# Kernel tuning notes

Hardware: AMD Instinct MI355X
Metric: run time of the kernel (lower is better)

## Reference

```python
import jax, jax.numpy as jnp
import numpy as np

D = 512      # d_model
H = 8        # nhead
HD = D // H  # head dim
L = 8        # axis-0 length (torch seq dim, batch_first=False)
S = 128      # axis-1 length (torch batch dim; relation-tensor axis)
NL = 3       # encoder layers
EPS = 1e-5


def setup_inputs() -> dict:
    key = jax.random.key(0)
    ks = jax.random.split(key, 16)
    w = lambda k, shape: jax.random.normal(k, shape, jnp.float32) * 0.02
    return {
        "x": jax.random.normal(ks[0], (L, S, D), jnp.float32),
        # stacked per-layer transformer params (leading dim = NL)
        "attn_in_w": w(ks[1], (NL, 3 * D, D)), "attn_in_b": jnp.zeros((NL, 3 * D), jnp.float32),
        "attn_out_w": w(ks[2], (NL, D, D)),    "attn_out_b": jnp.zeros((NL, D), jnp.float32),
        "ln1_w": jnp.ones((NL, D), jnp.float32), "ln1_b": jnp.zeros((NL, D), jnp.float32),
        "ln2_w": jnp.ones((NL, D), jnp.float32), "ln2_b": jnp.zeros((NL, D), jnp.float32),
        "ff1_w": w(ks[3], (NL, 4 * D, D)), "ff1_b": jnp.zeros((NL, 4 * D), jnp.float32),
        "ff2_w": w(ks[4], (NL, D, 4 * D)), "ff2_b": jnp.zeros((NL, D), jnp.float32),
        "fln_w": jnp.ones((D,), jnp.float32), "fln_b": jnp.zeros((D,), jnp.float32),
        # 4 projection MLPs stacked: 0=sub, 1=obj, 2=verb_sub, 3=verb_obj
        "mlp_w0": w(ks[5], (4, D, D)), "mlp_b0": jnp.zeros((4, D), jnp.float32),
        "mlp_w1": w(ks[6], (4, D, D)), "mlp_b1": jnp.zeros((4, D), jnp.float32),
        "mlp_w2": w(ks[7], (4, D, D)), "mlp_b2": jnp.zeros((4, D), jnp.float32),
    }


def _ln(x, w, b):
    m = jnp.mean(x, axis=-1, keepdims=True)
    v = jnp.mean(jnp.square(x - m), axis=-1, keepdims=True)
    return (x - m) * jax.lax.rsqrt(v + EPS) * w + b


def _mha(x, in_w, in_b, out_w, out_b):
    # x: (L, B, D); attention over axis 0 (torch batch_first=False semantics)
    l, b, _ = x.shape
    qkv = x @ in_w.T + in_b                      # (L, B, 3D)
    q, k, v = jnp.split(qkv, 3, axis=-1)
    q = q.reshape(l, b, H, HD)
    k = k.reshape(l, b, H, HD)
    v = v.reshape(l, b, H, HD)
    scores = jnp.einsum("lbhd,mbhd->bhlm", q, k) / jnp.sqrt(jnp.float32(HD))
    attn = jax.nn.softmax(scores, axis=-1)
    o = jnp.einsum("bhlm,mbhd->lbhd", attn, v).reshape(l, b, D)
    return o @ out_w.T + out_b


def _mlp(x, w0, b0, w1, b1, w2, b2):
    h = jax.nn.relu(x @ w0.T + b0)
    h = jax.nn.relu(h @ w1.T + b1)
    return h @ w2.T + b2


def _forward(x, attn_in_w, attn_in_b, attn_out_w, attn_out_b,
             ln1_w, ln1_b, ln2_w, ln2_b, ff1_w, ff1_b, ff2_w, ff2_b,
             fln_w, fln_b, mlp_w0, mlp_b0, mlp_w1, mlp_b1, mlp_w2, mlp_b2):
    # TransformerEncoder (post-norm, relu, no dropout at eval)
    h = x
    for i in range(NL):
        h = _ln(h + _mha(h, attn_in_w[i], attn_in_b[i], attn_out_w[i], attn_out_b[i]),
                ln1_w[i], ln1_b[i])
        ff = jax.nn.relu(h @ ff1_w[i].T + ff1_b[i]) @ ff2_w[i].T + ff2_b[i]
        h = _ln(h + ff, ln2_w[i], ln2_b[i])
    h = _ln(h, fln_w, fln_b)  # final encoder norm

    sub = _mlp(h, mlp_w0[0], mlp_b0[0], mlp_w1[0], mlp_b1[0], mlp_w2[0], mlp_b2[0])
    obj = _mlp(h, mlp_w0[1], mlp_b0[1], mlp_w1[1], mlp_b1[1], mlp_w2[1], mlp_b2[1])
    vsub = _mlp(h, mlp_w0[2], mlp_b0[2], mlp_w1[2], mlp_b1[2], mlp_w2[2], mlp_b2[2])
    vobj = _mlp(h, mlp_w0[3], mlp_b0[3], mlp_w1[3], mlp_b1[3], mlp_w2[3], mlp_b2[3])

    # sub.unsqueeze(1) * vsub.unsqueeze(2): (B0, S, S, D)
    sub4 = sub[:, None, :, :] * vsub[:, :, None, :]
    obj4 = obj[:, None, :, :] * vobj[:, :, None, :]
    # p_x = sub4 @ obj4.transpose(-2, -1): (B0, S, S, S)
    return jnp.einsum("bijd,bikd->bijk", sub4, obj4)


def reference(x, attn_in_w, attn_in_b, attn_out_w, attn_out_b,
              ln1_w, ln1_b, ln2_w, ln2_b, ff1_w, ff1_b, ff2_w, ff2_b,
              fln_w, fln_b, mlp_w0, mlp_b0, mlp_w1, mlp_b1, mlp_w2, mlp_b2):
    return _forward(x, attn_in_w, attn_in_b, attn_out_w, attn_out_b,
                    ln1_w, ln1_b, ln2_w, ln2_b, ff1_w, ff1_b, ff2_w, ff2_b,
                    fln_w, fln_b, mlp_w0, mlp_b0, mlp_w1, mlp_b1, mlp_w2, mlp_b2)
```

## Files before the change

### kernel.cpp

```cpp
#include <hip/hip_runtime.h>
#include <hip/hip_bf16.h>

#define DEV __device__ __forceinline__

typedef __attribute__((ext_vector_type(8))) short bf16x8;
typedef __attribute__((ext_vector_type(8))) unsigned short u16x8;
typedef __attribute__((ext_vector_type(4))) float f32x4;

DEV unsigned short f2bf(float f) {
  return __builtin_bit_cast(unsigned short, __float2bfloat16(f));
}
DEV float bf2f(unsigned short h) { return __uint_as_float(((unsigned int)h) << 16); }

DEV int swz(int row, int byteoff) { return row * 128 + (byteoff ^ ((row & 7) << 4)); }

__global__ void cvt_kernel(const float* __restrict__ src, unsigned short* __restrict__ dst,
                           float* __restrict__ dstf, int n) {
  long i = ((long)blockIdx.x * blockDim.x + threadIdx.x) * 8;
  long stride = (long)gridDim.x * blockDim.x * 8;
  for (; i < n; i += stride) {
    f32x4 a = *(const f32x4*)(src + i);
    f32x4 b = *(const f32x4*)(src + i + 4);
    u16x8 o;
    o[0] = f2bf(a[0]); o[1] = f2bf(a[1]); o[2] = f2bf(a[2]); o[3] = f2bf(a[3]);
    o[4] = f2bf(b[0]); o[5] = f2bf(b[1]); o[6] = f2bf(b[2]); o[7] = f2bf(b[3]);
    *(u16x8*)(dst + i) = o;
    if (dstf) { *(f32x4*)(dstf + i) = a; *(f32x4*)(dstf + i + 4) = b; }
  }
}

struct CvtJobs { const float* s[7]; unsigned short* d[7]; int n[7]; };
__global__ void cvtw_kernel(CvtJobs J) {
  const int seg = blockIdx.y;
  const float* __restrict__ src = J.s[seg];
  unsigned short* __restrict__ dst = J.d[seg];
  const int n = J.n[seg];
  long i = ((long)blockIdx.x * blockDim.x + threadIdx.x) * 8;
  long stride = (long)gridDim.x * blockDim.x * 8;
  for (; i < n; i += stride) {
    f32x4 a = *(const f32x4*)(src + i);
    f32x4 b = *(const f32x4*)(src + i + 4);
    u16x8 o;
    o[0] = f2bf(a[0]); o[1] = f2bf(a[1]); o[2] = f2bf(a[2]); o[3] = f2bf(a[3]);
    o[4] = f2bf(b[0]); o[5] = f2bf(b[1]); o[6] = f2bf(b[2]); o[7] = f2bf(b[3]);
    *(u16x8*)(dst + i) = o;
  }
}

template <int BM, int ACT, int WF32, int WBF>
__global__ __launch_bounds__(256) void gemm_kernel(
    const unsigned short* __restrict__ X, const unsigned short* __restrict__ Wt,
    const float* __restrict__ bias, float* Yf, unsigned short* __restrict__ Ybf,
    int M, int N, int K, long xbs, long wbs, long bbs, long ybs) {
  constexpr int CA = (BM * 64) / (256 * 8);
  constexpr int ABY = BM * 64 * 2;
  constexpr int BBY = 64 * 64 * 2;
  constexpr int MI = BM / 32;
  __shared__ __align__(16) char Asb[2 * ABY];
  __shared__ __align__(16) char Bsb[2 * BBY];
  const int t = threadIdx.x;
  const int bn = blockIdx.x, bm = blockIdx.y, bz = blockIdx.z;
  const unsigned short* Xp = X + (long)bz * xbs;
  const unsigned short* Wp = Wt + (long)bz * wbs;

  const int lane = t & 63, wv = t >> 6;
  const int wr = wv >> 1, wc = wv & 1;
  f32x4 acc[MI][2] = {};

  int rowA[CA], slotA[CA], rowB[2], slotB[2];
#pragma unroll
  for (int c = 0; c < CA; ++c) { int id = c * 256 + t; rowA[c] = id >> 3; slotA[c] = id & 7; }
#pragma unroll
  for (int c = 0; c < 2; ++c) { int id = c * 256 + t; rowB[c] = id >> 3; slotB[c] = id & 7; }

  u16x8 ra[CA], rb[2];
  auto load = [&](int kt) {
#pragma unroll
    for (int c = 0; c < CA; ++c)
      ra[c] = *(const u16x8*)(Xp + (long)(bm * BM + rowA[c]) * K + kt + slotA[c] * 8);
#pragma unroll
    for (int c = 0; c < 2; ++c)
      rb[c] = *(const u16x8*)(Wp + (long)(bn * 64 + rowB[c]) * K + kt + slotB[c] * 8);
  };
  auto store = [&](int cur) {
#pragma unroll
    for (int c = 0; c < CA; ++c)
      *(u16x8*)(Asb + cur * ABY + swz(rowA[c], slotA[c] * 16)) = ra[c];
#pragma unroll
    for (int c = 0; c < 2; ++c)
      *(u16x8*)(Bsb + cur * BBY + swz(rowB[c], slotB[c] * 16)) = rb[c];
  };

  const int NT = K >> 6;
  load(0);
  store(0);
  load(64);
  __syncthreads();
  for (int ki = 0; ki < NT; ++ki) {
    const int cur = ki & 1;
    if (ki + 1 < NT) store(cur ^ 1);
    if (ki + 2 < NT) load((ki + 2) << 6);
#pragma unroll
    for (int kk = 0; kk < 2; ++kk) {
      const int kb = kk * 64 + ((lane >> 4) << 4);
      bf16x8 af[MI], bfv[2];
#pragma unroll
      for (int mi = 0; mi < MI; ++mi)
        af[mi] = *(const bf16x8*)(Asb + cur * ABY + swz(wr * (MI * 16) + mi * 16 + (lane & 15), kb));
#pragma unroll
      for (int ni = 0; ni < 2; ++ni)
        bfv[ni] = *(const bf16x8*)(Bsb + cur * BBY + swz(wc * 32 + ni * 16 + (lane & 15), kb));
#pragma unroll
      for (int mi = 0; mi < MI; ++mi)
#pragma unroll
        for (int ni = 0; ni < 2; ++ni)
          acc[mi][ni] = __builtin_amdgcn_mfma_f32_16x16x32_bf16(af[mi], bfv[ni], acc[mi][ni], 0, 0, 0);
    }
    __syncthreads();
  }
#pragma unroll
  for (int ni = 0; ni < 2; ++ni) {
    const int n = bn * 64 + wc * 32 + ni * 16 + (lane & 15);
    const float bv = bias[(long)bz * bbs + n];
#pragma unroll
    for (int mi = 0; mi < MI; ++mi) {
#pragma unroll
      for (int rr = 0; rr < 4; ++rr) {
        const int gm = bm * BM + wr * (MI * 16) + mi * 16 + ((lane >> 4) << 2) + rr;
        float v = acc[mi][ni][rr] + bv;
        if (ACT == 1) v = fmaxf(v, 0.f);
        const long o = (long)bz * ybs + (long)gm * N + n;
        if (WF32) Yf[o] = v;
        if (WBF) Ybf[o] = f2bf(v);
      }
    }
  }
}

__global__ __launch_bounds__(256) void attn_kernel(const unsigned short* __restrict__ qkv,
                                                   unsigned short* __restrict__ o) {
  __shared__ float P[512];
  const int s = blockIdx.x;
  const int t = threadIdx.x;
#pragma unroll
  for (int rep = 0; rep < 2; ++rep) {
    const int idx = t + rep * 256;
    const int h = idx >> 6, l = (idx >> 3) & 7, m = idx & 7;
    const unsigned short* qp = qkv + (long)(l * 128 + s) * 1536 + h * 64;
    const unsigned short* kp = qkv + (long)(m * 128 + s) * 1536 + 512 + h * 64;
    float acc = 0.f;
#pragma unroll
    for (int c = 0; c < 64; c += 8) {
      u16x8 q8 = *(const u16x8*)(qp + c);
      u16x8 k8 = *(const u16x8*)(kp + c);
#pragma unroll
      for (int j = 0; j < 8; ++j) acc += bf2f(q8[j]) * bf2f(k8[j]);
    }
    P[idx] = acc * 0.125f;
  }
  __syncthreads();
  if (t < 64) {
    const int base = t * 8;
    float mx = -1e30f;
#pragma unroll
    for (int m = 0; m < 8; ++m) mx = fmaxf(mx, P[base + m]);
    float e[8], sum = 0.f;
#pragma unroll
    for (int m = 0; m < 8; ++m) { e[m] = expf(P[base + m] - mx); sum += e[m]; }
    const float inv = 1.f / sum;
#pragma unroll
    for (int m = 0; m < 8; ++m) P[base + m] = e[m] * inv;
  }
  __syncthreads();
#pragma unroll
  for (int rep = 0; rep < 16; ++rep) {
    const int idx = t + rep * 256;
    const int d = idx & 63, h = (idx >> 6) & 7, l = idx >> 9;
    float acc = 0.f;
#pragma unroll
    for (int m = 0; m < 8; ++m)
      acc += P[h * 64 + l * 8 + m] * bf2f(qkv[(long)(m * 128 + s) * 1536 + 1024 + h * 64 + d]);
    o[(long)(l * 128 + s) * 512 + h * 64 + d] = f2bf(acc);
  }
}

template <int RES, int WF32>
__global__ __launch_bounds__(256) void ln_kernel(const float* a, const float* res,
                                                 const float* __restrict__ w,
                                                 const float* __restrict__ bb, float* hf,
                                                 unsigned short* __restrict__ hbf) {
  __shared__ float red[8];
  const int row = blockIdx.x, t = threadIdx.x;
  const long base = (long)row * 512;
  float x0 = a[base + t], x1 = a[base + t + 256];
  if (RES) { x0 += res[base + t]; x1 += res[base + t + 256]; }
  float s = x0 + x1;
#pragma unroll
  for (int msk = 32; msk; msk >>= 1) s += __shfl_xor(s, msk, 64);
  if ((t & 63) == 0) red[t >> 6] = s;
  __syncthreads();
  const float mean = (red[0] + red[1] + red[2] + red[3]) * (1.f / 512.f);
  const float d0 = x0 - mean, d1 = x1 - mean;
  float v = d0 * d0 + d1 * d1;
#pragma unroll
  for (int msk = 32; msk; msk >>= 1) v += __shfl_xor(v, msk, 64);
  if ((t & 63) == 0) red[4 + (t >> 6)] = v;
  __syncthreads();
  const float var = (red[4] + red[5] + red[6] + red[7]) * (1.f / 512.f);
  const float inv = rsqrtf(var + 1e-5f);
  const float o0 = d0 * inv * w[t] + bb[t];
  const float o1 = d1 * inv * w[t + 256] + bb[t + 256];
  if (WF32) { hf[base + t] = o0; hf[base + t + 256] = o1; }
  hbf[base + t] = f2bf(o0);
  hbf[base + t + 256] = f2bf(o1);
}

__global__ __launch_bounds__(256) void phasec_kernel(const float* __restrict__ subp,
                                                     const unsigned short* __restrict__ objbf,
                                                     const float* __restrict__ vsub,
                                                     const float* __restrict__ vobj,
                                                     float* __restrict__ out) {
  constexpr int ABY = 128 * 64 * 2;
  __shared__ __align__(16) char Asb[2 * ABY];
  __shared__ __align__(16) char Bsb[2 * ABY];
  __shared__ float Wl[512];
  const int t = threadIdx.x;
  const int i = blockIdx.x, b = blockIdx.y;
  const long base_bi = ((long)b * 128 + i) * 512;
  for (int d = t; d < 512; d += 256) Wl[d] = vsub[base_bi + d] * vobj[base_bi + d];

  const int lane = t & 63, wv = t >> 6;
  const int wr = wv >> 1, wc = wv & 1;
  f32x4 acc[4][4] = {};

  int row[4], slot[4];
#pragma unroll
  for (int c = 0; c < 4; ++c) { int id = c * 256 + t; row[c] = id >> 3; slot[c] = id & 7; }

  f32x4 fa[4][2];
  u16x8 rb[4];
  auto load = [&](int kt) {
#pragma unroll
    for (int c = 0; c < 4; ++c) {
      const long g = ((long)b * 128 + row[c]) * 512 + kt + slot[c] * 8;
      fa[c][0] = *(const f32x4*)(subp + g);
      fa[c][1] = *(const f32x4*)(subp + g + 4);
      rb[c] = *(const u16x8*)(objbf + g);
    }
  };
  auto store = [&](int cur, int ktd) {
#pragma unroll
    for (int c = 0; c < 4; ++c) {
      const float* wp = Wl + ktd + slot[c] * 8;
      f32x4 w0 = *(const f32x4*)wp;
      f32x4 w1 = *(const f32x4*)(wp + 4);
      u16x8 oa;
      oa[0] = f2bf(fa[c][0][0] * w0[0]); oa[1] = f2bf(fa[c][0][1] * w0[1]);
      oa[2] = f2bf(fa[c][0][2] * w0[2]); oa[3] = f2bf(fa[c][0][3] * w0[3]);
      oa[4] = f2bf(fa[c][1][0] * w1[0]); oa[5] = f2bf(fa[c][1][1] * w1[1]);
      oa[6] = f2bf(fa[c][1][2] * w1[2]); oa[7] = f2bf(fa[c][1][3] * w1[3]);
      *(u16x8*)(Asb + cur * ABY + swz(row[c], slot[c] * 16)) = oa;
      *(u16x8*)(Bsb + cur * ABY + swz(row[c], slot[c] * 16)) = rb[c];
    }
  };

  __syncthreads();
  load(0);
  store(0, 0);
  load(64);
  __syncthreads();
  for (int ki = 0; ki < 8; ++ki) {
    const int cur = ki & 1;
    if (ki + 1 < 8) store(cur ^ 1, (ki + 1) * 64);
    if (ki + 2 < 8) load((ki + 2) * 64);
#pragma unroll
    for (int kk = 0; kk < 2; ++kk) {
      const int kb = kk * 64 + ((lane >> 4) << 4);
      bf16x8 af[4], bfv[4];
#pragma unroll
      for (int mi = 0; mi < 4; ++mi)
        af[mi] = *(const bf16x8*)(Asb + cur * ABY + swz(wr * 64 + mi * 16 + (lane & 15), kb));
#pragma unroll
      for (int ni = 0; ni < 4; ++ni)
        bfv[ni] = *(const bf16x8*)(Bsb + cur * ABY + swz(wc * 64 + ni * 16 + (lane & 15), kb));
#pragma unroll
      for (int mi = 0; mi < 4; ++mi)
#pragma unroll
        for (int ni = 0; ni < 4; ++ni)
          acc[mi][ni] = __builtin_amdgcn_mfma_f32_16x16x32_bf16(af[mi], bfv[ni], acc[mi][ni], 0, 0, 0);
    }
    __syncthreads();
  }
  float* ob = out + ((long)b * 128 + i) * 128 * 128;
#pragma unroll
  for (int mi = 0; mi < 4; ++mi) {
#pragma unroll
    for (int rr = 0; rr < 4; ++rr) {
      const int j = wr * 64 + mi * 16 + ((lane >> 4) << 2) + rr;
      float* orow = ob + (long)j * 128 + wc * 64 + (lane & 15);
#pragma unroll
      for (int ni = 0; ni < 4; ++ni) orow[ni * 16] = acc[mi][ni][rr];
    }
  }
}

extern "C" void kernel_launch(void* const* d_in, const int* in_sizes, int n_in, void* d_out,
                              int out_size, void* d_ws, size_t ws_size, hipStream_t stream) {
  const float* x          = (const float*)d_in[0];
  const float* attn_in_w  = (const float*)d_in[1];
  const float* attn_in_b  = (const float*)d_in[2];
  const float* attn_out_w = (const float*)d_in[3];
  const float* attn_out_b = (const float*)d_in[4];
  const float* ln1_w = (const float*)d_in[5];
  const float* ln1_b = (const float*)d_in[6];
  const float* ln2_w = (const float*)d_in[7];
  const float* ln2_b = (const float*)d_in[8];
  const float* ff1_w = (const float*)d_in[9];
  const float* ff1_b = (const float*)d_in[10];
  const float* ff2_w = (const float*)d_in[11];
  const float* ff2_b = (const float*)d_in[12];
  const float* fln_w = (const float*)d_in[13];
  const float* fln_b = (const float*)d_in[14];
  const float* mlp_w0 = (const float*)d_in[15];
  const float* mlp_b0 = (const float*)d_in[16];
  const float* mlp_w1 = (const float*)d_in[17];
  const float* mlp_b1 = (const float*)d_in[18];
  const float* mlp_w2 = (const float*)d_in[19];
  const float* mlp_b2 = (const float*)d_in[20];
  float* out = (float*)d_out;
  (void)in_sizes; (void)n_in; (void)out_size; (void)ws_size;

  char* ws = (char*)d_ws;
  size_t off = 0;
  auto alloc = [&](size_t bytes) -> void* {
    void* p = (void*)(ws + off);
    off += (bytes + 255) & ~(size_t)255;
    return p;
  };
  unsigned short* wq  = (unsigned short*)alloc((size_t)3 * 1536 * 512 * 2);
  unsigned short* wo  = (unsigned short*)alloc((size_t)3 * 512 * 512 * 2);
  unsigned short* wf1 = (unsigned short*)alloc((size_t)3 * 2048 * 512 * 2);
  unsigned short* wf2 = (unsigned short*)alloc((size_t)3 * 512 * 2048 * 2);
  unsigned short* wm0 = (unsigned short*)alloc((size_t)4 * 512 * 512 * 2);
  unsigned short* wm1 = (unsigned short*)alloc((size_t)4 * 512 * 512 * 2);
  unsigned short* wm2 = (unsigned short*)alloc((size_t)4 * 512 * 512 * 2);
  float* h            = (float*)alloc((size_t)1024 * 512 * 4);
  unsigned short* hbf = (unsigned short*)alloc((size_t)1024 * 512 * 2);
  unsigned short* t1  = (unsigned short*)alloc((size_t)1024 * 2048 * 2);
  float* t2           = (float*)alloc((size_t)1024 * 512 * 4);
  unsigned short* ao  = (unsigned short*)alloc((size_t)1024 * 512 * 2);
  unsigned short* z1  = (unsigned short*)alloc((size_t)4 * 1024 * 512 * 2);
  unsigned short* z2  = (unsigned short*)alloc((size_t)4 * 1024 * 512 * 2);
  float* hf4          = (float*)alloc((size_t)4 * 1024 * 512 * 4);
  unsigned short* hb4 = (unsigned short*)alloc((size_t)4 * 1024 * 512 * 2);

  CvtJobs J;
  J.s[0] = attn_in_w;  J.d[0] = wq;  J.n[0] = 3 * 1536 * 512;
  J.s[1] = attn_out_w; J.d[1] = wo;  J.n[1] = 3 * 512 * 512;
  J.s[2] = ff1_w;      J.d[2] = wf1; J.n[2] = 3 * 2048 * 512;
  J.s[3] = ff2_w;      J.d[3] = wf2; J.n[3] = 3 * 512 * 2048;
  J.s[4] = mlp_w0;     J.d[4] = wm0; J.n[4] = 4 * 512 * 512;
  J.s[5] = mlp_w1;     J.d[5] = wm1; J.n[5] = 4 * 512 * 512;
  J.s[6] = mlp_w2;     J.d[6] = wm2; J.n[6] = 4 * 512 * 512;
  cvtw_kernel<<<dim3(512, 7), 256, 0, stream>>>(J);
  cvt_kernel<<<256, 256, 0, stream>>>(x, hbf, h, 1024 * 512);

  for (int i = 0; i < 3; ++i) {
    gemm_kernel<64, 0, 0, 1><<<dim3(24, 16, 1), 256, 0, stream>>>(
        hbf, wq + (long)i * 1536 * 512, attn_in_b + i * 1536, nullptr, t1, 1024, 1536, 512, 0, 0, 0, 0);
    attn_kernel<<<128, 256, 0, stream>>>(t1, ao);
    gemm_kernel<32, 0, 1, 0><<<dim3(8, 32, 1), 256, 0, stream>>>(
        ao, wo + (long)i * 512 * 512, attn_out_b + i * 512, t2, nullptr, 1024, 512, 512, 0, 0, 0, 0);
    ln_kernel<1, 1><<<1024, 256, 0, stream>>>(t2, h, ln1_w + i * 512, ln1_b + i * 512, h, hbf);
    gemm_kernel<64, 1, 0, 1><<<dim3(32, 16, 1), 256, 0, stream>>>(
        hbf, wf1 + (long)i * 2048 * 512, ff1_b + i * 2048, nullptr, t1, 1024, 2048, 512, 0, 0, 0, 0);
    gemm_kernel<32, 0, 1, 0><<<dim3(8, 32, 1), 256, 0, stream>>>(
        t1, wf2 + (long)i * 512 * 2048, ff2_b + i * 512, t2, nullptr, 1024, 512, 2048, 0, 0, 0, 0);
    ln_kernel<1, 1><<<1024, 256, 0, stream>>>(t2, h, ln2_w + i * 512, ln2_b + i * 512, h, hbf);
  }
  ln_kernel<0, 0><<<1024, 256, 0, stream>>>(h, nullptr, fln_w, fln_b, h, hbf);

  gemm_kernel<32, 1, 0, 1><<<dim3(8, 32, 4), 256, 0, stream>>>(
      hbf, wm0, mlp_b0, nullptr, z1, 1024, 512, 512, 0, 512 * 512, 512, 1024 * 512);
  gemm_kernel<32, 1, 0, 1><<<dim3(8, 32, 4), 256, 0, stream>>>(
      z1, wm1, mlp_b1, nullptr, z2, 1024, 512, 512, 1024 * 512, 512 * 512, 512, 1024 * 512);
  gemm_kernel<32, 0, 1, 1><<<dim3(8, 32, 4), 256, 0, stream>>>(
      z2, wm2, mlp_b2, hf4, hb4, 1024, 512, 512, 1024 * 512, 512 * 512, 512, 1024 * 512);

  phasec_kernel<<<dim3(128, 8), 256, 0, stream>>>(
      hf4, hb4 + 1 * 1024 * 512, hf4 + 2L * 1024 * 512, hf4 + 3L * 1024 * 512, out);
}
```

Measured before the change: 379.6 us.

## Fuse out-proj/FF2 GEMMs with residual LayerNorm and stage phasec output through LDS

Adds a gemm_ln kernel where each block computes a full 32x512 row tile, so the residual add, bias and LayerNorm (plus the final encoder norm in the last layer) run in the GEMM epilogue. This removes the separate LN launches and the fp32 t2 round trip. The cost is that these GEMMs now launch only 32 blocks, which lowers parallelism, especially for the K=2048 FF2 step. It also merges the input conversion into the weight-conversion launch and stages the phasec output tile through LDS for coalesced float4 stores.

```diff
diff --git a/kernel.cpp b/kernel.cpp
--- a/kernel.cpp
+++ b/kernel.cpp
@@ -13,9 +13,15 @@
 DEV float bf2f(unsigned short h) { return __uint_as_float(((unsigned int)h) << 16); }
 
 DEV int swz(int row, int byteoff) { return row * 128 + (byteoff ^ ((row & 7) << 4)); }
-
-__global__ void cvt_kernel(const float* __restrict__ src, unsigned short* __restrict__ dst,
-                           float* __restrict__ dstf, int n) {
+DEV int swz32(int row, int slot) { return row * 64 + ((slot ^ ((row >> 1) & 3)) << 4); }
+
+struct CvtJobs { const float* s[8]; unsigned short* d[8]; float* df[8]; int n[8]; };
+__global__ void cvtw_kernel(CvtJobs J) {
+  const int seg = blockIdx.y;
+  const float* __restrict__ src = J.s[seg];
+  unsigned short* __restrict__ dst = J.d[seg];
+  float* __restrict__ dstf = J.df[seg];
+  const int n = J.n[seg];
   long i = ((long)blockIdx.x * blockDim.x + threadIdx.x) * 8;
   long stride = (long)gridDim.x * blockDim.x * 8;
   for (; i < n; i += stride) {
@@ -26,24 +32,6 @@
     o[4] = f2bf(b[0]); o[5] = f2bf(b[1]); o[6] = f2bf(b[2]); o[7] = f2bf(b[3]);
     *(u16x8*)(dst + i) = o;
     if (dstf) { *(f32x4*)(dstf + i) = a; *(f32x4*)(dstf + i + 4) = b; }
-  }
-}
-
-struct CvtJobs { const float* s[7]; unsigned short* d[7]; int n[7]; };
-__global__ void cvtw_kernel(CvtJobs J) {
-  const int seg = blockIdx.y;
-  const float* __restrict__ src = J.s[seg];
-  unsigned short* __restrict__ dst = J.d[seg];
-  const int n = J.n[seg];
-  long i = ((long)blockIdx.x * blockDim.x + threadIdx.x) * 8;
-  long stride = (long)gridDim.x * blockDim.x * 8;
-  for (; i < n; i += stride) {
-    f32x4 a = *(const f32x4*)(src + i);
-    f32x4 b = *(const f32x4*)(src + i + 4);
-    u16x8 o;
-    o[0] = f2bf(a[0]); o[1] = f2bf(a[1]); o[2] = f2bf(a[2]); o[3] = f2bf(a[3]);
-    o[4] = f2bf(b[0]); o[5] = f2bf(b[1]); o[6] = f2bf(b[2]); o[7] = f2bf(b[3]);
-    *(u16x8*)(dst + i) = o;
   }
 }
 
@@ -137,6 +125,175 @@
   }
 }
 
+template <int DOUBLE>
+__global__ __launch_bounds__(256) void gemm_ln_kernel(
+    const unsigned short* __restrict__ X, const unsigned short* __restrict__ Wt,
+    const float* __restrict__ bias, float* __restrict__ h,
+    unsigned short* __restrict__ hbf,
+    const float* __restrict__ g1, const float* __restrict__ b1,
+    const float* __restrict__ g2, const float* __restrict__ b2, int K) {
+  constexpr int ABY = 32 * 32 * 2;
+  constexpr int BBY = 512 * 32 * 2;
+  __shared__ __align__(16) char Asb[2 * ABY];
+  __shared__ __align__(16) char Bsb[2 * BBY];
+  __shared__ float RedS[4][32], RedQ[4][32], RedS2[4][32], RedQ2[4][32];
+  const int t = threadIdx.x;
+  const int bm = blockIdx.x;
+  const int lane = t & 63, wv = t >> 6;
+  f32x4 acc[2][8] = {};
+
+  const int arow = t >> 2, aslot = t & 3;
+  u16x8 ra, rbv[8];
+  auto load = [&](int kt) {
+    if (t < 128) ra = *(const u16x8*)(X + (long)(bm * 32 + arow) * K + kt + aslot * 8);
+#pragma unroll
+    for (int c = 0; c < 8; ++c) {
+      const int id = c * 256 + t, row = id >> 2, slot = id & 3;
+      rbv[c] = *(const u16x8*)(Wt + (long)row * K + kt + slot * 8);
+    }
+  };
+  auto store = [&](int cur) {
+    if (t < 128) *(u16x8*)(Asb + cur * ABY + swz32(arow, aslot)) = ra;
+#pragma unroll
+    for (int c = 0; c < 8; ++c) {
+      const int id = c * 256 + t, row = id >> 2, slot = id & 3;
+      *(u16x8*)(Bsb + cur * BBY + swz32(row, slot)) = rbv[c];
+    }
+  };
+
+  const int NT = K >> 5;
+  load(0);
+  store(0);
+  load(32);
+  __syncthreads();
+  for (int ki = 0; ki < NT; ++ki) {
+    const int cur = ki & 1;
+    if (ki + 1 < NT) store(cur ^ 1);
+    if (ki + 2 < NT) load((ki + 2) << 5);
+    const int ks = lane >> 4;
+    bf16x8 af[2];
+#pragma unroll
+    for (int mi = 0; mi < 2; ++mi)
+      af[mi] = *(const bf16x8*)(Asb + cur * ABY + swz32(mi * 16 + (lane & 15), ks));
+#pragma unroll
+    for (int ni = 0; ni < 8; ++ni) {
+      bf16x8 bfv = *(const bf16x8*)(Bsb + cur * BBY + swz32(wv * 128 + ni * 16 + (lane & 15), ks));
+#pragma unroll
+      for (int mi = 0; mi < 2; ++mi)
+        acc[mi][ni] = __builtin_amdgcn_mfma_f32_16x16x32_bf16(af[mi], bfv, acc[mi][ni], 0, 0, 0);
+    }
+    __syncthreads();
+  }
+
+  float ls[2][4], lq[2][4];
+#pragma unroll
+  for (int mi = 0; mi < 2; ++mi)
+#pragma unroll
+    for (int rr = 0; rr < 4; ++rr) {
+      const int gm = bm * 32 + mi * 16 + ((lane >> 4) << 2) + rr;
+      float s = 0.f, q = 0.f;
+#pragma unroll
+      for (int ni = 0; ni < 8; ++ni) {
+        const int col = wv * 128 + ni * 16 + (lane & 15);
+        float v = acc[mi][ni][rr] + bias[col] + h[(long)gm * 512 + col];
+        acc[mi][ni][rr] = v;
+        s += v; q += v * v;
+      }
+      ls[mi][rr] = s; lq[mi][rr] = q;
+    }
+#pragma unroll
+  for (int msk = 1; msk < 16; msk <<= 1)
+#pragma unroll
+    for (int mi = 0; mi < 2; ++mi)
+#pragma unroll
+      for (int rr = 0; rr < 4; ++rr) {
+        ls[mi][rr] += __shfl_xor(ls[mi][rr], msk, 64);
+        lq[mi][rr] += __shfl_xor(lq[mi][rr], msk, 64);
+      }
+  if ((lane & 15) == 0) {
+#pragma unroll
+    for (int mi = 0; mi < 2; ++mi)
+#pragma unroll
+      for (int rr = 0; rr < 4; ++rr) {
+        const int r = mi * 16 + ((lane >> 4) << 2) + rr;
+        RedS[wv][r] = ls[mi][rr];
+        RedQ[wv][r] = lq[mi][rr];
+      }
+  }
+  __syncthreads();
+#pragma unroll
+  for (int mi = 0; mi < 2; ++mi)
+#pragma unroll
+    for (int rr = 0; rr < 4; ++rr) {
+      const int r = mi * 16 + ((lane >> 4) << 2) + rr;
+      const float S = RedS[0][r] + RedS[1][r] + RedS[2][r] + RedS[3][r];
+      const float Q = RedQ[0][r] + RedQ[1][r] + RedQ[2][r] + RedQ[3][r];
+      const float mean = S * (1.f / 512.f);
+      const float var = Q * (1.f / 512.f) - mean * mean;
+      const float inv = rsqrtf(var + 1e-5f);
+      float s2 = 0.f, q2 = 0.f;
+#pragma unroll
+      for (int ni = 0; ni < 8; ++ni) {
+        const int col = wv * 128 + ni * 16 + (lane & 15);
+        float o1 = (acc[mi][ni][rr] - mean) * inv * g1[col] + b1[col];
+        acc[mi][ni][rr] = o1;
+        s2 += o1; q2 += o1 * o1;
+      }
+      ls[mi][rr] = s2; lq[mi][rr] = q2;
+    }
+  if (DOUBLE) {
+#pragma unroll
+    for (int msk = 1; msk < 16; msk <<= 1)
+#pragma unroll
+      for (int mi = 0; mi < 2; ++mi)
+#pragma unroll
+        for (int rr = 0; rr < 4; ++rr) {
+          ls[mi][rr] += __shfl_xor(ls[mi][rr], msk, 64);
+          lq[mi][rr] += __shfl_xor(lq[mi][rr], msk, 64);
+        }
+    if ((lane & 15) == 0) {
+#pragma unroll
+      for (int mi = 0; mi < 2; ++mi)
+#pragma unroll
+        for (int rr = 0; rr < 4; ++rr) {
+          const int r = mi * 16 + ((lane >> 4) << 2) + rr;
+          RedS2[wv][r] = ls[mi][rr];
+          RedQ2[wv][r] = lq[mi][rr];
+        }
+    }
+    __syncthreads();
+#pragma unroll
+    for (int mi = 0; mi < 2; ++mi)
+#pragma unroll
+      for (int rr = 0; rr < 4; ++rr) {
+        const int r = mi * 16 + ((lane >> 4) << 2) + rr;
+        const float S = RedS2[0][r] + RedS2[1][r] + RedS2[2][r] + RedS2[3][r];
+        const float Q = RedQ2[0][r] + RedQ2[1][r] + RedQ2[2][r] + RedQ2[3][r];
+        const float mean = S * (1.f / 512.f);
+        const float var = Q * (1.f / 512.f) - mean * mean;
+        const float inv = rsqrtf(var + 1e-5f);
+#pragma unroll
+        for (int ni = 0; ni < 8; ++ni) {
+          const int col = wv * 128 + ni * 16 + (lane & 15);
+          acc[mi][ni][rr] = (acc[mi][ni][rr] - mean) * inv * g2[col] + b2[col];
+        }
+      }
+  }
+#pragma unroll
+  for (int mi = 0; mi < 2; ++mi)
+#pragma unroll
+    for (int rr = 0; rr < 4; ++rr) {
+      const int gm = bm * 32 + mi * 16 + ((lane >> 4) << 2) + rr;
+#pragma unroll
+      for (int ni = 0; ni < 8; ++ni) {
+        const int col = wv * 128 + ni * 16 + (lane & 15);
+        const float v = acc[mi][ni][rr];
+        h[(long)gm * 512 + col] = v;
+        hbf[(long)gm * 512 + col] = f2bf(v);
+      }
+    }
+}
+
 __global__ __launch_bounds__(256) void attn_kernel(const unsigned short* __restrict__ qkv,
                                                    unsigned short* __restrict__ o) {
   __shared__ float P[512];
@@ -184,46 +341,16 @@
   }
 }
 
-template <int RES, int WF32>
-__global__ __launch_bounds__(256) void ln_kernel(const float* a, const float* res,
-                                                 const float* __restrict__ w,
-                                                 const float* __restrict__ bb, float* hf,
-                                                 unsigned short* __restrict__ hbf) {
-  __shared__ float red[8];
-  const int row = blockIdx.x, t = threadIdx.x;
-  const long base = (long)row * 512;
-  float x0 = a[base + t], x1 = a[base + t + 256];
-  if (RES) { x0 += res[base + t]; x1 += res[base + t + 256]; }
-  float s = x0 + x1;
-#pragma unroll
-  for (int msk = 32; msk; msk >>= 1) s += __shfl_xor(s, msk, 64);
-  if ((t & 63) == 0) red[t >> 6] = s;
-  __syncthreads();
-  const float mean = (red[0] + red[1] + red[2] + red[3]) * (1.f / 512.f);
-  const float d0 = x0 - mean, d1 = x1 - mean;
-  float v = d0 * d0 + d1 * d1;
-#pragma unroll
-  for (int msk = 32; msk; msk >>= 1) v += __shfl_xor(v, msk, 64);
-  if ((t & 63) == 0) red[4 + (t >> 6)] = v;
-  __syncthreads();
-  const float var = (red[4] + red[5] + red[6] + red[7]) * (1.f / 512.f);
-  const float inv = rsqrtf(var + 1e-5f);
-  const float o0 = d0 * inv * w[t] + bb[t];
-  const float o1 = d1 * inv * w[t + 256] + bb[t + 256];
-  if (WF32) { hf[base + t] = o0; hf[base + t + 256] = o1; }
-  hbf[base + t] = f2bf(o0);
-  hbf[base + t + 256] = f2bf(o1);
-}
-
 __global__ __launch_bounds__(256) void phasec_kernel(const float* __restrict__ subp,
                                                      const unsigned short* __restrict__ objbf,
                                                      const float* __restrict__ vsub,
                                                      const float* __restrict__ vobj,
                                                      float* __restrict__ out) {
   constexpr int ABY = 128 * 64 * 2;
-  __shared__ __align__(16) char Asb[2 * ABY];
-  __shared__ __align__(16) char Bsb[2 * ABY];
-  __shared__ float Wl[512];
+  __shared__ __align__(16) char SMEM[67584];
+  char* Asb = SMEM;
+  char* Bsb = SMEM + 2 * ABY;
+  float* Wl = (float*)(SMEM + 4 * ABY);
   const int t = threadIdx.x;
   const int i = blockIdx.x, b = blockIdx.y;
   const long base_bi = ((long)b * 128 + i) * 512;
@@ -291,16 +418,24 @@
     }
     __syncthreads();
   }
-  float* ob = out + ((long)b * 128 + i) * 128 * 128;
-#pragma unroll
-  for (int mi = 0; mi < 4; ++mi) {
+  float* C = (float*)SMEM;
+#pragma unroll
+  for (int mi = 0; mi < 4; ++mi)
 #pragma unroll
     for (int rr = 0; rr < 4; ++rr) {
       const int j = wr * 64 + mi * 16 + ((lane >> 4) << 2) + rr;
-      float* orow = ob + (long)j * 128 + wc * 64 + (lane & 15);
-#pragma unroll
-      for (int ni = 0; ni < 4; ++ni) orow[ni * 16] = acc[mi][ni][rr];
-    }
+      float* crow = C + j * 132 + wc * 64 + (lane & 15);
+#pragma unroll
+      for (int ni = 0; ni < 4; ++ni) crow[ni * 16] = acc[mi][ni][rr];
+    }
+  __syncthreads();
+  float* ob = out + ((long)b * 128 + i) * 128 * 128;
+  const int cc = (t & 31) * 4, jb = (t >> 5) * 16;
+#pragma unroll
+  for (int q = 0; q < 16; ++q) {
+    const int j = jb + q;
+    f32x4 v = *(const f32x4*)(C + j * 132 + cc);
+    *(f32x4*)(ob + (long)j * 128 + cc) = v;
   }
 }
 
@@ -347,7 +482,6 @@
   float* h            = (float*)alloc((size_t)1024 * 512 * 4);
   unsigned short* hbf = (unsigned short*)alloc((size_t)1024 * 512 * 2);
   unsigned short* t1  = (unsigned short*)alloc((size_t)1024 * 2048 * 2);
-  float* t2           = (float*)alloc((size_t)1024 * 512 * 4);
   unsigned short* ao  = (unsigned short*)alloc((size_t)1024 * 512 * 2);
   unsigned short* z1  = (unsigned short*)alloc((size_t)4 * 1024 * 512 * 2);
   unsigned short* z2  = (unsigned short*)alloc((size_t)4 * 1024 * 512 * 2);
@@ -355,6 +489,7 @@
   unsigned short* hb4 = (unsigned short*)alloc((size_t)4 * 1024 * 512 * 2);
 
   CvtJobs J;
+  for (int k = 0; k < 8; ++k) J.df[k] = nullptr;
   J.s[0] = attn_in_w;  J.d[0] = wq;  J.n[0] = 3 * 1536 * 512;
   J.s[1] = attn_out_w; J.d[1] = wo;  J.n[1] = 3 * 512 * 512;
   J.s[2] = ff1_w;      J.d[2] = wf1; J.n[2] = 3 * 2048 * 512;
@@ -362,23 +497,27 @@
   J.s[4] = mlp_w0;     J.d[4] = wm0; J.n[4] = 4 * 512 * 512;
   J.s[5] = mlp_w1;     J.d[5] = wm1; J.n[5] = 4 * 512 * 512;
   J.s[6] = mlp_w2;     J.d[6] = wm2; J.n[6] = 4 * 512 * 512;
-  cvtw_kernel<<<dim3(512, 7), 256, 0, stream>>>(J);
-  cvt_kernel<<<256, 256, 0, stream>>>(x, hbf, h, 1024 * 512);
+  J.s[7] = x;          J.d[7] = hbf; J.n[7] = 1024 * 512; J.df[7] = h;
+  cvtw_kernel<<<dim3(512, 8), 256, 0, stream>>>(J);
 
   for (int i = 0; i < 3; ++i) {
     gemm_kernel<64, 0, 0, 1><<<dim3(24, 16, 1), 256, 0, stream>>>(
         hbf, wq + (long)i * 1536 * 512, attn_in_b + i * 1536, nullptr, t1, 1024, 1536, 512, 0, 0, 0, 0);
     attn_kernel<<<128, 256, 0, stream>>>(t1, ao);
-    gemm_kernel<32, 0, 1, 0><<<dim3(8, 32, 1), 256, 0, stream>>>(
-        ao, wo + (long)i * 512 * 512, attn_out_b + i * 512, t2, nullptr, 1024, 512, 512, 0, 0, 0, 0);
-    ln_kernel<1, 1><<<1024, 256, 0, stream>>>(t2, h, ln1_w + i * 512, ln1_b + i * 512, h, hbf);
+    gemm_ln_kernel<0><<<32, 256, 0, stream>>>(
+        ao, wo + (long)i * 512 * 512, attn_out_b + i * 512, h, hbf,
+        ln1_w + i * 512, ln1_b + i * 512, nullptr, nullptr, 512);
     gemm_kernel<64, 1, 0, 1><<<dim3(32, 16, 1), 256, 0, stream>>>(
         hbf, wf1 + (long)i * 2048 * 512, ff1_b + i * 2048, nullptr, t1, 1024, 2048, 512, 0, 0, 0, 0);
-    gemm_kernel<32, 0, 1, 0><<<dim3(8, 32, 1), 256, 0, stream>>>(
-        t1, wf2 + (long)i * 512 * 2048, ff2_b + i * 512, t2, nullptr, 1024, 512, 2048, 0, 0, 0, 0);
-    ln_kernel<1, 1><<<1024, 256, 0, stream>>>(t2, h, ln2_w + i * 512, ln2_b + i * 512, h, hbf);
-  }
-  ln_kernel<0, 0><<<1024, 256, 0, stream>>>(h, nullptr, fln_w, fln_b, h, hbf);
+    if (i < 2)
+      gemm_ln_kernel<0><<<32, 256, 0, stream>>>(
+          t1, wf2 + (long)i * 512 * 2048, ff2_b + i * 512, h, hbf,
+          ln2_w + i * 512, ln2_b + i * 512, nullptr, nullptr, 2048);
+    else
+      gemm_ln_kernel<1><<<32, 256, 0, stream>>>(
+          t1, wf2 + (long)i * 512 * 2048, ff2_b + i * 512, h, hbf,
+          ln2_w + i * 512, ln2_b + i * 512, fln_w, fln_b, 2048);
+  }
 
   gemm_kernel<32, 1, 0, 1><<<dim3(8, 32, 4), 256, 0, stream>>>(
       hbf, wm0, mlp_b0, nullptr, z1, 1024, 512, 512, 0, 512 * 512, 512, 1024 * 512);
```

After: 489.4 us. 1.29x slower.
